# Optimization experiments

Hardware: AMD Instinct MI355X
Metric: run time of the kernel (lower is better)

## Reference

```python
import jax, jax.numpy as jnp
import numpy as np

B, H, W, C = 4, 128, 128, 256
HEADS, DHEAD = 8, 32


def conv2d(x, w, b=None, groups=1, pad=0):
    # x: [N,C,H,W], w: [O, C//groups, kh, kw]
    out = jax.lax.conv_general_dilated(
        x, w, window_strides=(1, 1), padding=[(pad, pad), (pad, pad)],
        dimension_numbers=("NCHW", "OIHW", "NCHW"), feature_group_count=groups)
    if b is not None:
        out = out + b[None, :, None, None]
    return out


def setup_inputs() -> dict:
    key = jax.random.key(0)
    ks = jax.random.split(key, 16)
    g = lambda i, shape, s=0.02: jax.random.normal(ks[i], shape, jnp.float32) * s
    return {
        "x": jax.random.normal(ks[0], (B, H, W, C), jnp.float32),
        "mask": jax.random.uniform(ks[1], (1, C, H, W), jnp.float32),
        "wq": g(2, (C, C)),
        "wk": g(3, (C, C)),
        "wv": g(4, (C, C)),
        "rescale": jnp.ones((HEADS, 1, 1), jnp.float32),
        "wproj": g(5, (C, C)),
        "bproj": jnp.zeros((C,), jnp.float32),
        "mg_w1": g(6, (C, C, 1, 1)),
        "mg_b1": jnp.zeros((C,), jnp.float32),
        "mg_w2": g(7, (C, C, 1, 1)),
        "mg_b2": jnp.zeros((C,), jnp.float32),
        "mg_dw": g(8, (C, 1, 5, 5)),
        "mg_db": jnp.zeros((C,), jnp.float32),
        "be_w1": g(9, (C, 1, 3, 3)),
        "be_w2": g(10, (C, 1, 3, 3)),
    }


def _l2norm(t, axis):
    n = jnp.sqrt(jnp.sum(t * t, axis=axis, keepdims=True))
    return t / jnp.maximum(n, 1e-12)


def reference(x, mask, wq, wk, wv, rescale, wproj, bproj,
              mg_w1, mg_b1, mg_w2, mg_b2, mg_dw, mg_db, be_w1, be_w2):
    b, h, w, c = x.shape
    heads = rescale.shape[0]
    d = c // heads
    n = h * w

    xf = x.reshape(b, n, c)
    q_inp = xf @ wq   # [b,n,c]
    k_inp = xf @ wk
    v_inp = xf @ wv

    # MaskGuidedMechanism (h==w so shift_back is identity)
    m = conv2d(mask, mg_w1, mg_b1)                                   # [1,c,h,w]
    attn_map = jax.nn.sigmoid(conv2d(conv2d(m, mg_w2, mg_b2), mg_dw, mg_db, groups=c, pad=2))
    m = m * attn_map + m
    mask_emb = jnp.transpose(m, (0, 2, 3, 1))                        # [1,h,w,c]
    ma = jnp.broadcast_to(mask_emb, (b, h, w, c)).reshape(b, n, c)

    split = lambda t: t.reshape(b, n, heads, d).transpose(0, 2, 1, 3)  # [b,heads,n,d]
    q, k, v, ma = map(split, (q_inp, k_inp, v_inp, ma))
    v = v * ma

    # channel attention: normalize over token dim n
    qn = _l2norm(q, axis=2)
    kn = _l2norm(k, axis=2)
    attn = jnp.einsum("bhni,bhnj->bhij", kn, qn)                     # [b,heads,d,d]
    attn = jax.nn.softmax(attn * rescale, axis=-1)
    out = jnp.einsum("bhij,bhnj->bhin", attn, v)                     # [b,heads,d,n]

    out = out.transpose(0, 3, 1, 2).reshape(b, n, heads * d)         # [b,n,c]
    out_c = (out @ wproj + bproj).reshape(b, h, w, c)

    # band_emb: depthwise3x3 -> GELU(exact) -> depthwise3x3 on v_inp image
    v_img = v_inp.reshape(b, h, w, c).transpose(0, 3, 1, 2)          # [b,c,h,w]
    y = conv2d(v_img, be_w1, groups=c, pad=1)
    y = jax.nn.gelu(y, approximate=False)
    y = conv2d(y, be_w2, groups=c, pad=1)
    out_p = y.transpose(0, 2, 3, 1)

    return out_c + out_p
```

## Files before the change

kernel.cpp:

```cpp
#include <hip/hip_runtime.h>
#include <stdint.h>

#define B 4
#define HW 128
#define C 256
#define NTOK 16384
#define MALL 65536
#define HEADS 8
#define DH 32

typedef float f32x4 __attribute__((ext_vector_type(4)));
typedef short s16x8 __attribute__((ext_vector_type(8)));
typedef short s16x4 __attribute__((ext_vector_type(4)));
typedef __bf16 bf16x8 __attribute__((ext_vector_type(8)));

__device__ __forceinline__ float bf2f(unsigned short u) {
  union { unsigned int i; float f; } x;
  x.i = ((unsigned int)u) << 16;
  return x.f;
}
__device__ __forceinline__ unsigned short f2bf(float f) {
  union { float f; unsigned int i; } x;
  x.f = f;
  unsigned int lsb = (x.i >> 16) & 1u;
  unsigned int r = x.i + 0x7fffu + lsb;
  return (unsigned short)(r >> 16);
}

__device__ __forceinline__ void gload_lds16(const void* g, void* l) {
  auto gp = reinterpret_cast<const __attribute__((address_space(1))) unsigned int*>(
      reinterpret_cast<uintptr_t>(g));
  auto lp = reinterpret_cast<__attribute__((address_space(3))) unsigned int*>(
      reinterpret_cast<uintptr_t>(l));
  __builtin_amdgcn_global_load_lds(gp, lp, 16, 0, 0);
}

#define CFENCE asm volatile("" ::: "memory")
#define LDSBAR()                                        \
  do {                                                  \
    asm volatile("s_waitcnt lgkmcnt(0)" ::: "memory");  \
    __builtin_amdgcn_s_barrier();                       \
    CFENCE;                                             \
  } while (0)

__global__ __launch_bounds__(256) void prep_w_kernel(
    const float* __restrict__ wq, const float* __restrict__ wk, const float* __restrict__ wv,
    const float* __restrict__ wproj, const float* __restrict__ w1, const float* __restrict__ w2,
    unsigned short* __restrict__ wqkvT, unsigned short* __restrict__ wprojT,
    unsigned short* __restrict__ w1b, unsigned short* __restrict__ w2b) {
  const int idx = blockIdx.x * 256 + threadIdx.x;
  const int mat = blockIdx.y;
  const int n = idx >> 8, k = idx & 255;
  switch (mat) {
    case 0: wqkvT[idx] = f2bf(wq[k * 256 + n]); break;
    case 1: wqkvT[65536 + idx] = f2bf(wk[k * 256 + n]); break;
    case 2: wqkvT[131072 + idx] = f2bf(wv[k * 256 + n]); break;
    case 3: wprojT[idx] = f2bf(wproj[k * 256 + n]); break;
    case 4: w1b[idx] = f2bf(w1[idx]); break;
    case 5: w2b[idx] = f2bf(w2[idx]); break;
  }
}

__global__ __launch_bounds__(1024) void tmask_kernel(const float* __restrict__ mask,
                                                     unsigned short* __restrict__ mT) {
  __shared__ float tile[32][33];
  const int p0 = blockIdx.x * 32, c0 = blockIdx.y * 32;
  const int tx = threadIdx.x & 31, ty = threadIdx.x >> 5;
  tile[ty][tx] = mask[(size_t)(c0 + ty) * NTOK + p0 + tx];
  __syncthreads();
  mT[(size_t)(p0 + ty) * C + c0 + tx] = f2bf(tile[tx][ty]);
}

__global__ __launch_bounds__(512) void gemm256_qkv_kernel(
    const float* __restrict__ X, const unsigned short* __restrict__ Bt,
    unsigned short* __restrict__ q, unsigned short* __restrict__ k,
    unsigned short* __restrict__ v) {
  __shared__ alignas(16) unsigned short smem[32768];
  unsigned short* lAb = smem;
  unsigned short* lBb = smem + 16384;
  const int nwg = gridDim.x;
  const int bid = blockIdx.x;
  const int qd = nwg >> 3, rr = nwg & 7;
  const int xcd = bid & 7, sidx = bid >> 3;
  const int swz = (xcd < rr ? xcd * (qd + 1) : rr * (qd + 1) + (xcd - rr) * qd) + sidx;
  const int m0 = (swz / 3) * 256;
  const int n0 = (swz % 3) * 256;
  const int t = threadIdx.x;
  const int w = t >> 6, l = t & 63;
  const int wr = w >> 2, wc = w & 3;
  const int lr = l & 15, lg = l >> 4;

  const int srow = t >> 2;
  const int ssl = (t & 3) ^ ((t >> 3) & 3);

  f32x4 va0, va1, va2, va3;
  auto ALOAD = [&](int kt) {
    const float* s0 = X + (size_t)(m0 + srow) * 256 + kt * 32 + ssl * 8;
    const float* s1 = X + (size_t)(m0 + 128 + srow) * 256 + kt * 32 + ssl * 8;
    va0 = *(const f32x4*)s0;
    va1 = *(const f32x4*)(s0 + 4);
    va2 = *(const f32x4*)s1;
    va3 = *(const f32x4*)(s1 + 4);
  };
  auto AWRITE = [&](int buf) {
    s16x8 o0, o1;
#pragma unroll
    for (int e = 0; e < 4; ++e) {
      o0[e] = (short)f2bf(va0[e]);
      o0[e + 4] = (short)f2bf(va1[e]);
      o1[e] = (short)f2bf(va2[e]);
      o1[e + 4] = (short)f2bf(va3[e]);
    }
    char* d = (char*)(lAb + buf * 8192);
    *(s16x8*)(d + t * 16) = o0;
    *(s16x8*)(d + 8192 + t * 16) = o1;
  };
  auto STAGEB = [&](int kt, int buf) {
    unsigned short* d = lBb + buf * 8192;
    const size_t kb = ((size_t)kt * 32 + ssl * 8) * 2;
    gload_lds16((const char*)Bt + ((size_t)(n0 + srow) * 256) * 2 + kb, (char*)d + t * 16);
    gload_lds16((const char*)Bt + ((size_t)(n0 + 128 + srow) * 256) * 2 + kb,
                (char*)d + 8192 + t * 16);
  };

  f32x4 acc[8][4];
#pragma unroll
  for (int m = 0; m < 8; ++m)
#pragma unroll
    for (int j = 0; j < 4; ++j) acc[m][j] = f32x4{0.f, 0.f, 0.f, 0.f};

  const int asl = (lg ^ ((lr >> 1) & 3)) * 8;
  const int aoff = lr * 32 + asl;
  const int awb = wr * 4096;
  const int boff = (wc >> 1) * 4096 + ((wc & 1) * 64 + lr) * 32 + asl;

  ALOAD(0);
  STAGEB(0, 0);
  asm volatile("s_waitcnt vmcnt(0)" ::: "memory");
  AWRITE(0);
  LDSBAR();

#pragma unroll
  for (int kt = 0; kt < 8; ++kt) {
    const int cur = kt & 1;
    const unsigned short* bufA = lAb + cur * 8192;
    const unsigned short* bufB = lBb + cur * 8192;
    bf16x8 bfr[4], af[4], af2[4];
#pragma unroll
    for (int j = 0; j < 4; ++j) bfr[j] = *(const bf16x8*)&bufB[boff + j * 512];
#pragma unroll
    for (int m = 0; m < 4; ++m) af[m] = *(const bf16x8*)&bufA[awb + aoff + m * 512];
#pragma unroll
    for (int m = 0; m < 4; ++m) af2[m] = *(const bf16x8*)&bufA[awb + aoff + (m + 4) * 512];
    if (kt < 7) {
      ALOAD(kt + 1);
      STAGEB(kt + 1, cur ^ 1);
    }
    __builtin_amdgcn_s_setprio(1);
#pragma unroll
    for (int m = 0; m < 4; ++m)
#pragma unroll
      for (int j = 0; j < 4; ++j)
        acc[m][j] = __builtin_amdgcn_mfma_f32_16x16x32_bf16(af[m], bfr[j], acc[m][j], 0, 0, 0);
#pragma unroll
    for (int m = 0; m < 4; ++m)
#pragma unroll
      for (int j = 0; j < 4; ++j)
        acc[m + 4][j] =
            __builtin_amdgcn_mfma_f32_16x16x32_bf16(af2[m], bfr[j], acc[m + 4][j], 0, 0, 0);
    __builtin_amdgcn_s_setprio(0);
    if (kt < 7) {
      asm volatile("s_waitcnt vmcnt(0)" ::: "memory");
      AWRITE(cur ^ 1);
    }
    LDSBAR();
  }

  unsigned short* dst = (n0 < 256) ? q : (n0 < 512 ? k : v);
  unsigned short* eph = smem;
#pragma unroll
  for (int c = 0; c < 4; ++c) {
    LDSBAR();
    if (wr == (c >> 1)) {
#pragma unroll
      for (int mm = 0; mm < 4; ++mm) {
        const int m = (c & 1) * 4 + mm;
        const int lrow = mm * 16 + lg * 4;
#pragma unroll
        for (int j = 0; j < 4; ++j) {
          const int col = wc * 64 + j * 16 + lr;
#pragma unroll
          for (int r = 0; r < 4; ++r) eph[(lrow + r) * 264 + col] = f2bf(acc[m][j][r]);
        }
      }
    }
    LDSBAR();
    const int col16 = t & 31;
#pragma unroll
    for (int c2 = 0; c2 < 4; ++c2) {
      const int lrow = c2 * 16 + (t >> 5);
      const int grow = m0 + c * 64 + lrow;
      const s16x8 vv = *(const s16x8*)&eph[lrow * 264 + col16 * 8];
      *(s16x8*)&dst[(size_t)grow * C + col16 * 8] = vv;
    }
  }
}

__global__ __launch_bounds__(512) void gemm256_proj_kernel(
    const unsigned short* __restrict__ V, const unsigned short* __restrict__ memb,
    const unsigned short* __restrict__ weff, const float* __restrict__ bias,
    const unsigned short* __restrict__ y2, float* __restrict__ out) {
  __shared__ alignas(16) unsigned short smem[32768];
  unsigned short* lAb = smem;
  unsigned short* lBb = smem + 16384;
  const int nwg = gridDim.x;
  const int bid = blockIdx.x;
  const int qd = nwg >> 3, rr = nwg & 7;
  const int xcd = bid & 7, sidx = bid >> 3;
  const int swz = (xcd < rr ? xcd * (qd + 1) : rr * (qd + 1) + (xcd - rr) * qd) + sidx;
  const int m0 = swz * 256;
  const unsigned short* Bt = weff + (size_t)(m0 >> 14) * 65536;
  const int t = threadIdx.x;
  const int w = t >> 6, l = t & 63;
  const int wr = w >> 2, wc = w & 3;
  const int lr = l & 15, lg = l >> 4;

  const int srow = t >> 2;
  const int ssl = (t & 3) ^ ((t >> 3) & 3);
  const size_t mrow = (size_t)((m0 & 16383) + srow);

  s16x8 va0, va1, ma0, ma1;
  auto ALOAD = [&](int kt) {
    const int ko = kt * 32 + ssl * 8;
    va0 = *(const s16x8*)&V[(size_t)(m0 + srow) * 256 + ko];
    ma0 = *(const s16x8*)&memb[mrow * 256 + ko];
    va1 = *(const s16x8*)&V[(size_t)(m0 + 128 + srow) * 256 + ko];
    ma1 = *(const s16x8*)&memb[(mrow + 128) * 256 + ko];
  };
  auto AWRITE = [&](int buf) {
    s16x8 o0, o1;
#pragma unroll
    for (int e = 0; e < 8; ++e) {
      o0[e] = (short)f2bf(bf2f((unsigned short)va0[e]) * bf2f((unsigned short)ma0[e]));
      o1[e] = (short)f2bf(bf2f((unsigned short)va1[e]) * bf2f((unsigned short)ma1[e]));
    }
    char* d = (char*)(lAb + buf * 8192);
    *(s16x8*)(d + t * 16) = o0;
    *(s16x8*)(d + 8192 + t * 16) = o1;
  };
  auto STAGEB = [&](int kt, int buf) {
    unsigned short* d = lBb + buf * 8192;
    const size_t kb = ((size_t)kt * 32 + ssl * 8) * 2;
    gload_lds16((const char*)Bt + ((size_t)srow * 256) * 2 + kb, (char*)d + t * 16);
    gload_lds16((const char*)Bt + ((size_t)(128 + srow) * 256) * 2 + kb,
                (char*)d + 8192 + t * 16);
  };

  f32x4 acc[8][4];
#pragma unroll
  for (int m = 0; m < 8; ++m)
#pragma unroll
    for (int j = 0; j < 4; ++j) acc[m][j] = f32x4{0.f, 0.f, 0.f, 0.f};

  const int asl = (lg ^ ((lr >> 1) & 3)) * 8;
  const int aoff = lr * 32 + asl;
  const int awb = wr * 4096;
  const int boff = (wc >> 1) * 4096 + ((wc & 1) * 64 + lr) * 32 + asl;

  ALOAD(0);
  STAGEB(0, 0);
  asm volatile("s_waitcnt vmcnt(0)" ::: "memory");
  AWRITE(0);
  LDSBAR();

#pragma unroll
  for (int kt = 0; kt < 8; ++kt) {
    const int cur = kt & 1;
    const unsigned short* bufA = lAb + cur * 8192;
    const unsigned short* bufB = lBb + cur * 8192;
    bf16x8 bfr[4], af[4], af2[4];
#pragma unroll
    for (int j = 0; j < 4; ++j) bfr[j] = *(const bf16x8*)&bufB[boff + j * 512];
#pragma unroll
    for (int m = 0; m < 4; ++m) af[m] = *(const bf16x8*)&bufA[awb + aoff + m * 512];
#pragma unroll
    for (int m = 0; m < 4; ++m) af2[m] = *(const bf16x8*)&bufA[awb + aoff + (m + 4) * 512];
    if (kt < 7) {
      ALOAD(kt + 1);
      STAGEB(kt + 1, cur ^ 1);
    }
    __builtin_amdgcn_s_setprio(1);
#pragma unroll
    for (int m = 0; m < 4; ++m)
#pragma unroll
      for (int j = 0; j < 4; ++j)
        acc[m][j] = __builtin_amdgcn_mfma_f32_16x16x32_bf16(af[m], bfr[j], acc[m][j], 0, 0, 0);
#pragma unroll
    for (int m = 0; m < 4; ++m)
#pragma unroll
      for (int j = 0; j < 4; ++j)
        acc[m + 4][j] =
            __builtin_amdgcn_mfma_f32_16x16x32_bf16(af2[m], bfr[j], acc[m + 4][j], 0, 0, 0);
    __builtin_amdgcn_s_setprio(0);
    if (kt < 7) {
      asm volatile("s_waitcnt vmcnt(0)" ::: "memory");
      AWRITE(cur ^ 1);
    }
    LDSBAR();
  }

  float* ephf = (float*)smem;
  const int colc = t & 63;
  const f32x4 bv = *(const f32x4*)&bias[colc * 4];
#pragma unroll
  for (int c = 0; c < 8; ++c) {
    LDSBAR();
    if (wr == (c >> 2)) {
#pragma unroll
      for (int mm = 0; mm < 2; ++mm) {
        const int m = (c & 3) * 2 + mm;
        const int lrow = mm * 16 + lg * 4;
#pragma unroll
        for (int j = 0; j < 4; ++j) {
          const int col = wc * 64 + j * 16 + lr;
#pragma unroll
          for (int r = 0; r < 4; ++r) ephf[(lrow + r) * 260 + col] = acc[m][j][r];
        }
      }
    }
    LDSBAR();
#pragma unroll
    for (int c2 = 0; c2 < 4; ++c2) {
      const int lrow = c2 * 8 + (t >> 6);
      const int grow = m0 + c * 32 + lrow;
      const f32x4 vv = *(const f32x4*)&ephf[lrow * 260 + colc * 4];
      const s16x4 yv = *(const s16x4*)&y2[(size_t)grow * C + colc * 4];
      f32x4 o;
#pragma unroll
      for (int e = 0; e < 4; ++e) o[e] = vv[e] + bv[e] + bf2f((unsigned short)yv[e]);
      *(f32x4*)&out[(size_t)grow * C + colc * 4] = o;
    }
  }
}

__global__ __launch_bounds__(256) void gemm_bt_kernel(
    const unsigned short* __restrict__ A, const unsigned short* __restrict__ Bt, const int K,
    const int nbn, const int mode, unsigned short* __restrict__ ob0,
    const float* __restrict__ bias) {
  __shared__ unsigned short lA[2][128 * 64];
  __shared__ unsigned short lB[2][128 * 64];
  const int nwg = gridDim.x;
  const int bid = blockIdx.x;
  const int qd = nwg >> 3, rr = nwg & 7;
  const int xcd = bid & 7, sidx = bid >> 3;
  const int swz = (xcd < rr ? xcd * (qd + 1) : rr * (qd + 1) + (xcd - rr) * qd) + sidx;
  const int m0 = (swz / nbn) * 128;
  const int n0 = (swz % nbn) * 128;
  const int t = threadIdx.x;
  const int w = t >> 6, l = t & 63;
  const int wr = w >> 1, wc = w & 1;
  const int lr = l & 15, lg = l >> 4;

  const int strow = (l >> 3);
  const int scolb = (((l & 7) ^ strow) << 4);

  f32x4 acc[4][4];
#pragma unroll
  for (int i = 0; i < 4; ++i)
#pragma unroll
    for (int j = 0; j < 4; ++j) acc[i][j] = f32x4{0.f, 0.f, 0.f, 0.f};

  auto stage = [&](int buf, int k0) {
#pragma unroll
    for (int s = 0; s < 4; ++s) {
      const int seg = w * 4 + s;
      const int row = seg * 8 + strow;
      gload_lds16((const char*)A + ((size_t)(m0 + row) * K + k0) * 2 + scolb,
                  (char*)&lA[buf][0] + seg * 1024 + (l & 7) * 16);
      gload_lds16((const char*)Bt + ((size_t)(n0 + row) * K + k0) * 2 + scolb,
                  (char*)&lB[buf][0] + seg * 1024 + (l & 7) * 16);
    }
  };
  auto compute = [&](int buf) {
#pragma unroll
    for (int kk = 0; kk < 64; kk += 32) {
      bf16x8 af[4], bfr[4];
      const int sbase = (kk >> 3) + lg;
      const int p = (sbase ^ (lr & 7)) << 3;
#pragma unroll
      for (int i = 0; i < 4; ++i)
        af[i] = *(const bf16x8*)&lA[buf][(wr * 64 + i * 16 + lr) * 64 + p];
#pragma unroll
      for (int j = 0; j < 4; ++j)
        bfr[j] = *(const bf16x8*)&lB[buf][(wc * 64 + j * 16 + lr) * 64 + p];
#pragma unroll
      for (int i = 0; i < 4; ++i)
#pragma unroll
        for (int j = 0; j < 4; ++j)
          acc[i][j] = __builtin_amdgcn_mfma_f32_16x16x32_bf16(af[i], bfr[j], acc[i][j], 0, 0, 0);
    }
  };

  stage(0, 0);
  __syncthreads();
  int cur = 0;
  for (int k0 = 64; k0 < K; k0 += 64) {
    stage(cur ^ 1, k0);
    compute(cur);
    __syncthreads();
    cur ^= 1;
  }
  compute(cur);

#pragma unroll
  for (int i = 0; i < 4; ++i) {
    const int grow = m0 + wr * 64 + i * 16 + lg * 4;
#pragma unroll
    for (int j = 0; j < 4; ++j) {
      const int gcol = n0 + wc * 64 + j * 16 + lr;
#pragma unroll
      for (int r = 0; r < 4; ++r) {
        const float v = acc[i][j][r];
        const size_t row = (size_t)(grow + r);
        ob0[row * C + gcol] = f2bf(v + bias[gcol]);
      }
    }
  }
}

__global__ __launch_bounds__(256) void mask_dw5_kernel(
    const unsigned short* __restrict__ m2, const unsigned short* __restrict__ m1,
    const float* __restrict__ dw, const float* __restrict__ db,
    unsigned short* __restrict__ memb) {
  __shared__ float wlds[25 * 256];
  __shared__ float blds[256];
  const int t = threadIdx.x;
  const int y = blockIdx.y;
  const int x0 = blockIdx.x * 16 + (t >> 6) * 4;
  const int cg = (t & 63) * 4;
#pragma unroll
  for (int e = 0; e < 25; ++e) wlds[e * 256 + t] = dw[t * 25 + e];
  blds[t] = db[t];
  __syncthreads();

  const f32x4 bias = *(const f32x4*)&blds[cg];
  f32x4 acc[4];
#pragma unroll
  for (int xi = 0; xi < 4; ++xi) acc[xi] = bias;

#pragma unroll
  for (int dy = 0; dy < 5; ++dy) {
    const int yy = y + dy - 2;
    if (yy < 0 || yy >= HW) continue;
    f32x4 col[8];
#pragma unroll
    for (int j = 0; j < 8; ++j) {
      const int xx = x0 - 2 + j;
      if (xx >= 0 && xx < HW) {
        const s16x4 v = *(const s16x4*)&m2[((size_t)yy * HW + xx) * C + cg];
        col[j][0] = bf2f((unsigned short)v[0]);
        col[j][1] = bf2f((unsigned short)v[1]);
        col[j][2] = bf2f((unsigned short)v[2]);
        col[j][3] = bf2f((unsigned short)v[3]);
      } else {
        col[j] = f32x4{0.f, 0.f, 0.f, 0.f};
      }
    }
#pragma unroll
    for (int dx = 0; dx < 5; ++dx) {
      const f32x4 wv = *(const f32x4*)&wlds[(dy * 5 + dx) * 256 + cg];
#pragma unroll
      for (int xi = 0; xi < 4; ++xi) acc[xi] += wv * col[dx + xi];
    }
  }

#pragma unroll
  for (int xi = 0; xi < 4; ++xi) {
    const size_t oi = ((size_t)y * HW + x0 + xi) * C + cg;
    const s16x4 mv = *(const s16x4*)&m1[oi];
    s16x4 o;
#pragma unroll
    for (int ch = 0; ch < 4; ++ch) {
      const float a = 1.f / (1.f + __expf(-acc[xi][ch]));
      o[ch] = (short)f2bf(bf2f((unsigned short)mv[ch]) * (1.f + a));
    }
    *(s16x4*)&memb[oi] = o;
  }
}

__global__ __launch_bounds__(256) void gram_kernel(const unsigned short* __restrict__ qb,
                                                   const unsigned short* __restrict__ kb,
                                                   float* __restrict__ Gpart,
                                                   float* __restrict__ ssq,
                                                   float* __restrict__ ssk) {
  const int chunk = blockIdx.x;
  const int h = blockIdx.y;
  const int b = blockIdx.z;
  __shared__ float flk[128 * 32], flq[128 * 32];
  const int t = threadIdx.x;
  const int wv = t >> 6;
  const int i0 = (t & 7) * 4, j0 = ((t >> 3) & 7) * 4;
  const int lrow = t >> 2, lcb = (t & 3) * 8;
  float acc[4][4] = {};
  float sq[8] = {}, sk[8] = {};
  for (int sub = 0; sub < 8; ++sub) {
    const size_t nbase = (size_t)b * NTOK + chunk * 1024 + sub * 128;
    __syncthreads();
#pragma unroll
    for (int it = 0; it < 2; ++it) {
      const int row = it * 64 + lrow;
      const s16x8 kv8 = *(const s16x8*)&kb[(nbase + row) * C + h * 32 + lcb];
      const s16x8 qv8 = *(const s16x8*)&qb[(nbase + row) * C + h * 32 + lcb];
      f32x4 ka, kbb, qa, qbb;
#pragma unroll
      for (int e = 0; e < 4; ++e) {
        ka[e] = bf2f((unsigned short)kv8[e]);
        kbb[e] = bf2f((unsigned short)kv8[e + 4]);
        qa[e] = bf2f((unsigned short)qv8[e]);
        qbb[e] = bf2f((unsigned short)qv8[e + 4]);
      }
#pragma unroll
      for (int e = 0; e < 4; ++e) {
        sk[e] += ka[e] * ka[e];
        sk[e + 4] += kbb[e] * kbb[e];
        sq[e] += qa[e] * qa[e];
        sq[e + 4] += qbb[e] * qbb[e];
      }
      *(f32x4*)&flk[row * 32 + lcb] = ka;
      *(f32x4*)&flk[row * 32 + lcb + 4] = kbb;
      *(f32x4*)&flq[row * 32 + lcb] = qa;
      *(f32x4*)&flq[row * 32 + lcb + 4] = qbb;
    }
    __syncthreads();
    for (int n = wv; n < 128; n += 4) {
      const f32x4 kv = *(const f32x4*)&flk[n * 32 + i0];
      const f32x4 qv = *(const f32x4*)&flq[n * 32 + j0];
#pragma unroll
      for (int a = 0; a < 4; ++a)
#pragma unroll
        for (int bb = 0; bb < 4; ++bb) acc[a][bb] += kv[a] * qv[bb];
    }
  }
  const int pc = chunk * 4 + wv;
  float* dst = Gpart + (((size_t)pc * B + b) * HEADS + h) * 1024;
#pragma unroll
  for (int a = 0; a < 4; ++a)
#pragma unroll
    for (int bb = 0; bb < 4; ++bb) dst[(i0 + a) * 32 + (j0 + bb)] = acc[a][bb];
  __syncthreads();
#pragma unroll
  for (int e = 0; e < 8; ++e) {
    flq[t * 8 + e] = sq[e];
    flk[t * 8 + e] = sk[e];
  }
  __syncthreads();
  if (t < 32) {
    const int tm = t >> 3, e = t & 7;
    float s1 = 0.f, s2 = 0.f;
    for (int k2 = 0; k2 < 64; ++k2) {
      const int tt = tm + k2 * 4;
      s1 += flq[tt * 8 + e];
      s2 += flk[tt * 8 + e];
    }
    ssq[((size_t)b * 16 + chunk) * C + h * 32 + t] = s1;
    ssk[((size_t)b * 16 + chunk) * C + h * 32 + t] = s2;
  }
}

__global__ __launch_bounds__(256) void softmax_kernel(
    const float* __restrict__ Gpart, const float* __restrict__ ssq,
    const float* __restrict__ ssk, const float* __restrict__ rescale,
    unsigned short* __restrict__ attnb) {
  const int h = blockIdx.x, b = blockIdx.y;
  const int t = threadIdx.x;
  __shared__ float G[1024];
  __shared__ float nq[32], nk[32];
#pragma unroll
  for (int e = 0; e < 4; ++e) {
    const int cell = e * 256 + t;
    float s = 0.f;
    for (int pc = 0; pc < 64; ++pc)
      s += Gpart[(((size_t)pc * B + b) * HEADS + h) * 1024 + cell];
    G[cell] = s;
  }
  if (t < 64) {
    const int d = t & 31;
    const float* ss = (t < 32) ? ssq : ssk;
    float s = 0.f;
    for (int ch = 0; ch < 16; ++ch) s += ss[((size_t)b * 16 + ch) * C + h * 32 + d];
    const float nn = fmaxf(sqrtf(s), 1e-12f);
    if (t < 32) nq[d] = nn;
    else nk[d] = nn;
  }
  __syncthreads();
  if (t < 32) {
    const int i = t;
    const float rs = rescale[h];
    float row[32];
    float mx = -1e30f;
#pragma unroll
    for (int j = 0; j < 32; ++j) {
      const float v = G[i * 32 + j] / (nk[i] * nq[j]) * rs;
      row[j] = v;
      mx = fmaxf(mx, v);
    }
    float sum = 0.f;
#pragma unroll
    for (int j = 0; j < 32; ++j) {
      const float e = expf(row[j] - mx);
      row[j] = e;
      sum += e;
    }
    const float inv = 1.f / sum;
#pragma unroll
    for (int j = 0; j < 32; ++j)
      attnb[(((size_t)b * HEADS + h) * 32 + i) * 32 + j] = f2bf(row[j] * inv);
  }
}

__global__ __launch_bounds__(256) void weff_kernel(const unsigned short* __restrict__ attnb,
                                                   const unsigned short* __restrict__ wprojT,
                                                   unsigned short* __restrict__ weff) {
  const int b = blockIdx.y;
  const int co0 = blockIdx.x * 64;
  const int t = threadIdx.x;
  __shared__ float att[8192];
  for (int e = t; e < 8192; e += 256) att[e] = bf2f(attnb[(size_t)b * 8192 + e]);
  __syncthreads();
  const int o = co0 + (t & 63);
  const int hq = t >> 6;
#pragma unroll
  for (int hh = 0; hh < 2; ++hh) {
    const int h = hq * 2 + hh;
    float wp[32];
#pragma unroll
    for (int i = 0; i < 32; ++i) wp[i] = bf2f(wprojT[(size_t)o * 256 + h * 32 + i]);
    for (int j4 = 0; j4 < 8; ++j4) {
      f32x4 s = {0.f, 0.f, 0.f, 0.f};
#pragma unroll
      for (int i = 0; i < 32; ++i) {
        const f32x4 a4 = *(const f32x4*)&att[(h * 32 + i) * 32 + j4 * 4];
        s += wp[i] * a4;
      }
      s16x4 oo;
#pragma unroll
      for (int e = 0; e < 4; ++e) oo[e] = (short)f2bf(s[e]);
      *(s16x4*)&weff[((size_t)b * 256 + o) * 256 + h * 32 + j4 * 4] = oo;
    }
  }
}

__global__ __launch_bounds__(512) void dw3_kernel(const unsigned short* __restrict__ in,
                                                  const float* __restrict__ wgt,
                                                  unsigned short* __restrict__ out_bf,
                                                  const int do_gelu) {
  const int y = blockIdx.x;
  const int b = blockIdx.y;
  const int t = threadIdx.x;
  const int cg = (t & 63) * 4;
  const int x0 = (t >> 6) * 16;
  float w[9][4];
#pragma unroll
  for (int e = 0; e < 9; ++e)
#pragma unroll
    for (int ch = 0; ch < 4; ++ch) w[e][ch] = wgt[(cg + ch) * 9 + e];
  const int ym = y - 1, yp = y + 1;
  const bool hm = (ym >= 0), hp = (yp < HW);
  const size_t base = (size_t)b * NTOK * C + cg;
  auto ld4 = [&](int yy, int xx) -> f32x4 {
    const s16x4 v = *(const s16x4*)&in[base + ((size_t)yy * HW + xx) * C];
    f32x4 f;
    f[0] = bf2f((unsigned short)v[0]);
    f[1] = bf2f((unsigned short)v[1]);
    f[2] = bf2f((unsigned short)v[2]);
    f[3] = bf2f((unsigned short)v[3]);
    return f;
  };
  const f32x4 zero = {0.f, 0.f, 0.f, 0.f};
  f32x4 a0, a1, a2, b0, b1, b2;
  if (x0 > 0) {
    a0 = hm ? ld4(ym, x0 - 1) : zero;
    a1 = ld4(y, x0 - 1);
    a2 = hp ? ld4(yp, x0 - 1) : zero;
  } else {
    a0 = a1 = a2 = zero;
  }
  b0 = hm ? ld4(ym, x0) : zero;
  b1 = ld4(y, x0);
  b2 = hp ? ld4(yp, x0) : zero;
  for (int xi = 0; xi < 16; ++xi) {
    const int x = x0 + xi;
    f32x4 c0, c1, c2;
    if (x + 1 < HW) {
      c0 = hm ? ld4(ym, x + 1) : zero;
      c1 = ld4(y, x + 1);
      c2 = hp ? ld4(yp, x + 1) : zero;
    } else {
      c0 = c1 = c2 = zero;
    }
    float res[4];
#pragma unroll
    for (int ch = 0; ch < 4; ++ch) {
      float r = w[0][ch] * a0[ch] + w[1][ch] * b0[ch] + w[2][ch] * c0[ch] +
                w[3][ch] * a1[ch] + w[4][ch] * b1[ch] + w[5][ch] * c1[ch] +
                w[6][ch] * a2[ch] + w[7][ch] * b2[ch] + w[8][ch] * c2[ch];
      if (do_gelu) r = 0.5f * r * (1.f + erff(r * 0.70710678118654752f));
      res[ch] = r;
    }
    const size_t oi = base + ((size_t)y * HW + x) * C;
    s16x4 o;
    o[0] = (short)f2bf(res[0]);
    o[1] = (short)f2bf(res[1]);
    o[2] = (short)f2bf(res[2]);
    o[3] = (short)f2bf(res[3]);
    *(s16x4*)&out_bf[oi] = o;
    a0 = b0; a1 = b1; a2 = b2;
    b0 = c0; b1 = c1; b2 = c2;
  }
}

extern "C" void kernel_launch(void* const* d_in, const int* in_sizes, int n_in, void* d_out,
                              int out_size, void* d_ws, size_t ws_size, hipStream_t stream) {
  (void)in_sizes; (void)n_in; (void)out_size; (void)ws_size;
  const float* x = (const float*)d_in[0];
  const float* maskp = (const float*)d_in[1];
  const float* wq = (const float*)d_in[2];
  const float* wk = (const float*)d_in[3];
  const float* wv = (const float*)d_in[4];
  const float* rescale = (const float*)d_in[5];
  const float* wproj = (const float*)d_in[6];
  const float* bproj = (const float*)d_in[7];
  const float* mg_w1 = (const float*)d_in[8];
  const float* mg_b1 = (const float*)d_in[9];
  const float* mg_w2 = (const float*)d_in[10];
  const float* mg_b2 = (const float*)d_in[11];
  const float* mg_dw = (const float*)d_in[12];
  const float* mg_db = (const float*)d_in[13];
  const float* be_w1 = (const float*)d_in[14];
  const float* be_w2 = (const float*)d_in[15];
  float* out = (float*)d_out;
  char* ws = (char*)d_ws;

  unsigned short* qb = (unsigned short*)(ws + 33554432ull);
  unsigned short* kb = (unsigned short*)(ws + 67108864ull);
  unsigned short* vb = (unsigned short*)(ws + 100663296ull);
  unsigned short* mT = (unsigned short*)(ws + 134217728ull);
  unsigned short* m1b = (unsigned short*)(ws + 142606336ull);
  unsigned short* m2b = (unsigned short*)(ws + 150994944ull);
  unsigned short* wqkvT = (unsigned short*)(ws + 159383552ull);
  unsigned short* wprojT = (unsigned short*)(ws + 159776768ull);
  unsigned short* w1b = (unsigned short*)(ws + 159907840ull);
  unsigned short* w2b = (unsigned short*)(ws + 160038912ull);
  float* ssq = (float*)(ws + 160169984ull);
  float* ssk = (float*)(ws + 160432128ull);
  unsigned short* attnb = (unsigned short*)(ws + 160694272ull);
  float* Gpart = (float*)m2b;
  unsigned short* memb = mT;
  unsigned short* y1 = qb;
  unsigned short* y2 = kb;
  unsigned short* weff = m1b;

  prep_w_kernel<<<dim3(256, 6), 256, 0, stream>>>(wq, wk, wv, wproj, mg_w1, mg_w2, wqkvT,
                                                  wprojT, w1b, w2b);
  tmask_kernel<<<dim3(512, 8), 1024, 0, stream>>>(maskp, mT);
  gemm_bt_kernel<<<256, 256, 0, stream>>>(mT, w1b, 256, 2, 1, m1b, mg_b1);
  gemm_bt_kernel<<<256, 256, 0, stream>>>(m1b, w2b, 256, 2, 1, m2b, mg_b2);
  mask_dw5_kernel<<<dim3(8, 128), 256, 0, stream>>>(m2b, m1b, mg_dw, mg_db, memb);
  gemm256_qkv_kernel<<<768, 512, 0, stream>>>(x, wqkvT, qb, kb, vb);
  gram_kernel<<<dim3(16, 8, 4), 256, 0, stream>>>(qb, kb, Gpart, ssq, ssk);
  softmax_kernel<<<dim3(8, 4), 256, 0, stream>>>(Gpart, ssq, ssk, rescale, attnb);
  weff_kernel<<<dim3(4, 4), 256, 0, stream>>>(attnb, wprojT, weff);
  dw3_kernel<<<dim3(128, 4), 512, 0, stream>>>(vb, be_w1, y1, 1);
  dw3_kernel<<<dim3(128, 4), 512, 0, stream>>>(y1, be_w2, y2, 0);
  gemm256_proj_kernel<<<256, 512, 0, stream>>>(vb, memb, weff, bproj, y2, out);
}
```

Measured before the change: 278.1 us.

## Pre-cast x to bf16 for async LDS loads; fuse two depthwise 3x3 convs

Adds a separate kernel that casts x to bf16 so the QKV GEMM can stage A through direct global-to-LDS loads, like B, instead of loading fp32 into registers and converting. It also fuses the two depthwise 3x3 convolutions with GELU into one tiled kernel that keeps the intermediate in LDS with a halo. This removes one full round trip of the intermediate through global memory. In exchange it adds an extra read and write pass over x, plus halo recompute in the fused conv.

```diff
diff --git a/kernel.cpp b/kernel.cpp
--- a/kernel.cpp
+++ b/kernel.cpp
@@ -36,12 +36,33 @@
 }
 
 #define CFENCE asm volatile("" ::: "memory")
+#define RAWBAR()                      \
+  do {                                \
+    CFENCE;                           \
+    __builtin_amdgcn_s_barrier();     \
+    CFENCE;                           \
+  } while (0)
 #define LDSBAR()                                        \
   do {                                                  \
     asm volatile("s_waitcnt lgkmcnt(0)" ::: "memory");  \
     __builtin_amdgcn_s_barrier();                       \
     CFENCE;                                             \
   } while (0)
+
+__global__ __launch_bounds__(256) void cast_x_kernel(const float* __restrict__ x,
+                                                     unsigned short* __restrict__ xb) {
+  const size_t stride = (size_t)gridDim.x * blockDim.x * 4;
+  for (size_t i = ((size_t)blockIdx.x * blockDim.x + threadIdx.x) * 4; i < (size_t)MALL * C;
+       i += stride) {
+    const float4 v = *(const float4*)&x[i];
+    s16x4 o;
+    o[0] = (short)f2bf(v.x);
+    o[1] = (short)f2bf(v.y);
+    o[2] = (short)f2bf(v.z);
+    o[3] = (short)f2bf(v.w);
+    *(s16x4*)&xb[i] = o;
+  }
+}
 
 __global__ __launch_bounds__(256) void prep_w_kernel(
     const float* __restrict__ wq, const float* __restrict__ wk, const float* __restrict__ wv,
@@ -72,7 +93,7 @@
 }
 
 __global__ __launch_bounds__(512) void gemm256_qkv_kernel(
-    const float* __restrict__ X, const unsigned short* __restrict__ Bt,
+    const unsigned short* __restrict__ A, const unsigned short* __restrict__ Bt,
     unsigned short* __restrict__ q, unsigned short* __restrict__ k,
     unsigned short* __restrict__ v) {
   __shared__ alignas(16) unsigned short smem[32768];
@@ -93,33 +114,18 @@
   const int srow = t >> 2;
   const int ssl = (t & 3) ^ ((t >> 3) & 3);
 
-  f32x4 va0, va1, va2, va3;
-  auto ALOAD = [&](int kt) {
-    const float* s0 = X + (size_t)(m0 + srow) * 256 + kt * 32 + ssl * 8;
-    const float* s1 = X + (size_t)(m0 + 128 + srow) * 256 + kt * 32 + ssl * 8;
-    va0 = *(const f32x4*)s0;
-    va1 = *(const f32x4*)(s0 + 4);
-    va2 = *(const f32x4*)s1;
-    va3 = *(const f32x4*)(s1 + 4);
+  auto stageA = [&](int kt) {
+    unsigned short* d = lAb + (kt & 1) * 8192;
+    const size_t kb2 = ((size_t)kt * 32 + ssl * 8) * 2;
+    gload_lds16((const char*)A + ((size_t)(m0 + srow) * 256) * 2 + kb2, (char*)d + t * 16);
+    gload_lds16((const char*)A + ((size_t)(m0 + 128 + srow) * 256) * 2 + kb2,
+                (char*)d + 8192 + t * 16);
   };
-  auto AWRITE = [&](int buf) {
-    s16x8 o0, o1;
-#pragma unroll
-    for (int e = 0; e < 4; ++e) {
-      o0[e] = (short)f2bf(va0[e]);
-      o0[e + 4] = (short)f2bf(va1[e]);
-      o1[e] = (short)f2bf(va2[e]);
-      o1[e + 4] = (short)f2bf(va3[e]);
-    }
-    char* d = (char*)(lAb + buf * 8192);
-    *(s16x8*)(d + t * 16) = o0;
-    *(s16x8*)(d + 8192 + t * 16) = o1;
-  };
-  auto STAGEB = [&](int kt, int buf) {
-    unsigned short* d = lBb + buf * 8192;
-    const size_t kb = ((size_t)kt * 32 + ssl * 8) * 2;
-    gload_lds16((const char*)Bt + ((size_t)(n0 + srow) * 256) * 2 + kb, (char*)d + t * 16);
-    gload_lds16((const char*)Bt + ((size_t)(n0 + 128 + srow) * 256) * 2 + kb,
+  auto stageB = [&](int kt) {
+    unsigned short* d = lBb + (kt & 1) * 8192;
+    const size_t kb2 = ((size_t)kt * 32 + ssl * 8) * 2;
+    gload_lds16((const char*)Bt + ((size_t)(n0 + srow) * 256) * 2 + kb2, (char*)d + t * 16);
+    gload_lds16((const char*)Bt + ((size_t)(n0 + 128 + srow) * 256) * 2 + kb2,
                 (char*)d + 8192 + t * 16);
   };
 
@@ -134,11 +140,9 @@
   const int awb = wr * 4096;
   const int boff = (wc >> 1) * 4096 + ((wc & 1) * 64 + lr) * 32 + asl;
 
-  ALOAD(0);
-  STAGEB(0, 0);
+  stageA(0); stageB(0);
   asm volatile("s_waitcnt vmcnt(0)" ::: "memory");
-  AWRITE(0);
-  LDSBAR();
+  RAWBAR();
 
 #pragma unroll
   for (int kt = 0; kt < 8; ++kt) {
@@ -152,10 +156,7 @@
     for (int m = 0; m < 4; ++m) af[m] = *(const bf16x8*)&bufA[awb + aoff + m * 512];
 #pragma unroll
     for (int m = 0; m < 4; ++m) af2[m] = *(const bf16x8*)&bufA[awb + aoff + (m + 4) * 512];
-    if (kt < 7) {
-      ALOAD(kt + 1);
-      STAGEB(kt + 1, cur ^ 1);
-    }
+    if (kt < 7) { stageA(kt + 1); stageB(kt + 1); }
     __builtin_amdgcn_s_setprio(1);
 #pragma unroll
     for (int m = 0; m < 4; ++m)
@@ -169,11 +170,8 @@
         acc[m + 4][j] =
             __builtin_amdgcn_mfma_f32_16x16x32_bf16(af2[m], bfr[j], acc[m + 4][j], 0, 0, 0);
     __builtin_amdgcn_s_setprio(0);
-    if (kt < 7) {
-      asm volatile("s_waitcnt vmcnt(0)" ::: "memory");
-      AWRITE(cur ^ 1);
-    }
-    LDSBAR();
+    if (kt < 7) asm volatile("s_waitcnt vmcnt(0)" ::: "memory");
+    RAWBAR();
   }
 
   unsigned short* dst = (n0 < 256) ? q : (n0 < 512 ? k : v);
@@ -250,9 +248,9 @@
   };
   auto STAGEB = [&](int kt, int buf) {
     unsigned short* d = lBb + buf * 8192;
-    const size_t kb = ((size_t)kt * 32 + ssl * 8) * 2;
-    gload_lds16((const char*)Bt + ((size_t)srow * 256) * 2 + kb, (char*)d + t * 16);
-    gload_lds16((const char*)Bt + ((size_t)(128 + srow) * 256) * 2 + kb,
+    const size_t kb2 = ((size_t)kt * 32 + ssl * 8) * 2;
+    gload_lds16((const char*)Bt + ((size_t)srow * 256) * 2 + kb2, (char*)d + t * 16);
+    gload_lds16((const char*)Bt + ((size_t)(128 + srow) * 256) * 2 + kb2,
                 (char*)d + 8192 + t * 16);
   };
 
@@ -650,25 +648,29 @@
   }
 }
 
-__global__ __launch_bounds__(512) void dw3_kernel(const unsigned short* __restrict__ in,
-                                                  const float* __restrict__ wgt,
-                                                  unsigned short* __restrict__ out_bf,
-                                                  const int do_gelu) {
-  const int y = blockIdx.x;
-  const int b = blockIdx.y;
+__global__ __launch_bounds__(256) void dw3x2_kernel(const unsigned short* __restrict__ vb,
+                                                    const float* __restrict__ w1,
+                                                    const float* __restrict__ w2,
+                                                    unsigned short* __restrict__ y2) {
+  __shared__ unsigned short y1l[18 * 18 * 64];
+  __shared__ float w1l[9 * 64], w2l[9 * 64];
+  const int x0 = blockIdx.x * 16;
+  const int y0 = blockIdx.y * 16;
+  const int b = blockIdx.z >> 2;
+  const int cg = (blockIdx.z & 3) * 64;
   const int t = threadIdx.x;
-  const int cg = (t & 63) * 4;
-  const int x0 = (t >> 6) * 16;
-  float w[9][4];
-#pragma unroll
-  for (int e = 0; e < 9; ++e)
-#pragma unroll
-    for (int ch = 0; ch < 4; ++ch) w[e][ch] = wgt[(cg + ch) * 9 + e];
-  const int ym = y - 1, yp = y + 1;
-  const bool hm = (ym >= 0), hp = (yp < HW);
-  const size_t base = (size_t)b * NTOK * C + cg;
-  auto ld4 = [&](int yy, int xx) -> f32x4 {
-    const s16x4 v = *(const s16x4*)&in[base + ((size_t)yy * HW + xx) * C];
+  const int chq = t & 15;
+  const int xl = t >> 4;
+  const int c4 = chq * 4;
+  for (int e = t; e < 576; e += 256) {
+    const int tap = e >> 6, ch = e & 63;
+    w1l[tap * 64 + ch] = w1[(cg + ch) * 9 + tap];
+    w2l[tap * 64 + ch] = w2[(cg + ch) * 9 + tap];
+  }
+  __syncthreads();
+  const size_t gbase = (size_t)b * NTOK * C + cg + c4;
+  auto ldv = [&](int yy, int xx) -> f32x4 {
+    const s16x4 v = *(const s16x4*)&vb[gbase + ((size_t)yy * HW + xx) * C];
     f32x4 f;
     f[0] = bf2f((unsigned short)v[0]);
     f[1] = bf2f((unsigned short)v[1]);
@@ -676,46 +678,54 @@
     f[3] = bf2f((unsigned short)v[3]);
     return f;
   };
-  const f32x4 zero = {0.f, 0.f, 0.f, 0.f};
-  f32x4 a0, a1, a2, b0, b1, b2;
-  if (x0 > 0) {
-    a0 = hm ? ld4(ym, x0 - 1) : zero;
-    a1 = ld4(y, x0 - 1);
-    a2 = hp ? ld4(yp, x0 - 1) : zero;
-  } else {
-    a0 = a1 = a2 = zero;
-  }
-  b0 = hm ? ld4(ym, x0) : zero;
-  b1 = ld4(y, x0);
-  b2 = hp ? ld4(yp, x0) : zero;
-  for (int xi = 0; xi < 16; ++xi) {
-    const int x = x0 + xi;
-    f32x4 c0, c1, c2;
-    if (x + 1 < HW) {
-      c0 = hm ? ld4(ym, x + 1) : zero;
-      c1 = ld4(y, x + 1);
-      c2 = hp ? ld4(yp, x + 1) : zero;
-    } else {
-      c0 = c1 = c2 = zero;
-    }
-    float res[4];
-#pragma unroll
-    for (int ch = 0; ch < 4; ++ch) {
-      float r = w[0][ch] * a0[ch] + w[1][ch] * b0[ch] + w[2][ch] * c0[ch] +
-                w[3][ch] * a1[ch] + w[4][ch] * b1[ch] + w[5][ch] * c1[ch] +
-                w[6][ch] * a2[ch] + w[7][ch] * b2[ch] + w[8][ch] * c2[ch];
-      if (do_gelu) r = 0.5f * r * (1.f + erff(r * 0.70710678118654752f));
-      res[ch] = r;
-    }
-    const size_t oi = base + ((size_t)y * HW + x) * C;
+  for (int pass = 0; pass < 2; ++pass) {
+    const int xi = pass ? (16 + xl) : xl;
+    if (pass && xl >= 2) break;
+    const int xg = x0 - 1 + xi;
+    for (int j = 0; j < 18; ++j) {
+      const int yg = y0 - 1 + j;
+      f32x4 acc = {0.f, 0.f, 0.f, 0.f};
+      if (xg >= 0 && xg < HW && yg >= 0 && yg < HW) {
+#pragma unroll
+        for (int dy = 0; dy < 3; ++dy) {
+          const int vy = yg + dy - 1;
+          if (vy < 0 || vy >= HW) continue;
+#pragma unroll
+          for (int dx = 0; dx < 3; ++dx) {
+            const int vx = xg + dx - 1;
+            if (vx < 0 || vx >= HW) continue;
+            const f32x4 wv = *(const f32x4*)&w1l[(dy * 3 + dx) * 64 + c4];
+            acc += wv * ldv(vy, vx);
+          }
+        }
+#pragma unroll
+        for (int e = 0; e < 4; ++e)
+          acc[e] = 0.5f * acc[e] * (1.f + erff(acc[e] * 0.70710678118654752f));
+      }
+      s16x4 o;
+#pragma unroll
+      for (int e = 0; e < 4; ++e) o[e] = (short)f2bf(acc[e]);
+      *(s16x4*)&y1l[(j * 18 + xi) * 64 + c4] = o;
+    }
+  }
+  __syncthreads();
+  for (int yo = 0; yo < 16; ++yo) {
+    f32x4 acc = {0.f, 0.f, 0.f, 0.f};
+#pragma unroll
+    for (int dy = 0; dy < 3; ++dy)
+#pragma unroll
+      for (int dx = 0; dx < 3; ++dx) {
+        const f32x4 wv = *(const f32x4*)&w2l[(dy * 3 + dx) * 64 + c4];
+        const s16x4 yv = *(const s16x4*)&y1l[((yo + dy) * 18 + xl + dx) * 64 + c4];
+        f32x4 yf;
+#pragma unroll
+        for (int e = 0; e < 4; ++e) yf[e] = bf2f((unsigned short)yv[e]);
+        acc += wv * yf;
+      }
     s16x4 o;
-    o[0] = (short)f2bf(res[0]);
-    o[1] = (short)f2bf(res[1]);
-    o[2] = (short)f2bf(res[2]);
-    o[3] = (short)f2bf(res[3]);
-    *(s16x4*)&out_bf[oi] = o;
-    a0 = b0; a1 = b1; a2 = b2;
-    b0 = c0; b1 = c1; b2 = c2;
+#pragma unroll
+    for (int e = 0; e < 4; ++e) o[e] = (short)f2bf(acc[e]);
+    *(s16x4*)&y2[gbase + ((size_t)(y0 + yo) * HW + x0 + xl) * C] = o;
   }
 }
 
@@ -741,6 +751,7 @@
   float* out = (float*)d_out;
   char* ws = (char*)d_ws;
 
+  unsigned short* xb = (unsigned short*)(ws + 0ull);
   unsigned short* qb = (unsigned short*)(ws + 33554432ull);
   unsigned short* kb = (unsigned short*)(ws + 67108864ull);
   unsigned short* vb = (unsigned short*)(ws + 100663296ull);
@@ -756,21 +767,20 @@
   unsigned short* attnb = (unsigned short*)(ws + 160694272ull);
   float* Gpart = (float*)m2b;
   unsigned short* memb = mT;
-  unsigned short* y1 = qb;
   unsigned short* y2 = kb;
   unsigned short* weff = m1b;
 
   prep_w_kernel<<<dim3(256, 6), 256, 0, stream>>>(wq, wk, wv, wproj, mg_w1, mg_w2, wqkvT,
                                                   wprojT, w1b, w2b);
   tmask_kernel<<<dim3(512, 8), 1024, 0, stream>>>(maskp, mT);
+  cast_x_kernel<<<2048, 256, 0, stream>>>(x, xb);
   gemm_bt_kernel<<<256, 256, 0, stream>>>(mT, w1b, 256, 2, 1, m1b, mg_b1);
   gemm_bt_kernel<<<256, 256, 0, stream>>>(m1b, w2b, 256, 2, 1, m2b, mg_b2);
   mask_dw5_kernel<<<dim3(8, 128), 256, 0, stream>>>(m2b, m1b, mg_dw, mg_db, memb);
-  gemm256_qkv_kernel<<<768, 512, 0, stream>>>(x, wqkvT, qb, kb, vb);
+  gemm256_qkv_kernel<<<768, 512, 0, stream>>>(xb, wqkvT, qb, kb, vb);
   gram_kernel<<<dim3(16, 8, 4), 256, 0, stream>>>(qb, kb, Gpart, ssq, ssk);
   softmax_kernel<<<dim3(8, 4), 256, 0, stream>>>(Gpart, ssq, ssk, rescale, attnb);
   weff_kernel<<<dim3(4, 4), 256, 0, stream>>>(attnb, wprojT, weff);
-  dw3_kernel<<<dim3(128, 4), 512, 0, stream>>>(vb, be_w1, y1, 1);
-  dw3_kernel<<<dim3(128, 4), 512, 0, stream>>>(y1, be_w2, y2, 0);
+  dw3x2_kernel<<<dim3(8, 8, 16), 256, 0, stream>>>(vb, be_w1, be_w2, y2);
   gemm256_proj_kernel<<<256, 512, 0, stream>>>(vb, memb, weff, bproj, y2, out);
 }
```

New measurement: 378.5 us. 36.1% more time.
